# Optimization experiments

Measured on AMD Instinct MI355X. Metric: run time of the kernel, lower is better.

Reference implementation:

```python
import jax, jax.numpy as jnp
import numpy as np

NUM_BLOCKS = 6
D_MODEL = 1024
D_FF = 4096
NUM_HEADS = 16
NIN = 32
SEQ = NIN + 1  # +1 for SOS/EOS slot in the order-respecting mask
BATCH = 1024
D_HEAD = D_MODEL // NUM_HEADS
NEG = 1e10


def _order_masks(n):
    # order_respecting_mask with natural ordering arange(n)
    m0 = np.zeros((n + 1, n + 1), np.int32)  # input-layer mask
    m0[:, 0] = 1
    for s in range(n):
        for d in range(s + 1, n):
            m0[d, s + 1] = 1
    m0[-1, :] = 0
    mr = np.zeros((n + 1, n + 1), np.int32)  # later-layer mask (sees self)
    for s in range(n):
        for d in range(s, n):
            mr[d, s] = 1
    return jnp.asarray(m0), jnp.asarray(mr)


def setup_inputs() -> dict:
    key = jax.random.key(0)
    ks = jax.random.split(key, 6)
    std = 0.02  # Conv1d init std
    L, D, F = NUM_BLOCKS, D_MODEL, D_FF
    m0, mr = _order_masks(NIN)
    return {
        "x": jax.random.normal(ks[0], (BATCH, SEQ, D), jnp.float32),
        "qkv_w": std * jax.random.normal(ks[1], (L, D, 3 * D), jnp.float32),
        "qkv_b": jnp.zeros((L, 3 * D), jnp.float32),
        "proj_w": std * jax.random.normal(ks[2], (L, D, D), jnp.float32),
        "proj_b": jnp.zeros((L, D), jnp.float32),
        "w1": std * jax.random.normal(ks[3], (L, D, F), jnp.float32),
        "b1": jnp.zeros((L, F), jnp.float32),
        "w2": std * jax.random.normal(ks[4], (L, F, D), jnp.float32),
        "b2": jnp.zeros((L, D), jnp.float32),
        "ln1_s": jnp.ones((L, D), jnp.float32),
        "ln1_b": jnp.zeros((L, D), jnp.float32),
        "ln2_s": jnp.ones((L, D), jnp.float32),
        "ln2_b": jnp.zeros((L, D), jnp.float32),
        "lnf_s": jnp.ones((D,), jnp.float32),
        "lnf_b": jnp.zeros((D,), jnp.float32),
        "mask0": m0,
        "mask_rest": mr,
    }


def _ln(h, scale, shift, eps=1e-5):
    mean = h.mean(-1, keepdims=True)
    var = jnp.mean((h - mean) ** 2, axis=-1, keepdims=True)
    return scale * ((h - mean) * jax.lax.rsqrt(var + eps)) + shift


def _forward(x, qkv_w, qkv_b, proj_w, proj_b, w1, b1, w2, b2,
             ln1_s, ln1_b, ln2_s, ln2_b, lnf_s, lnf_b, mask0, mask_rest):
    B, S, D = x.shape
    H, Dh = NUM_HEADS, D_HEAD
    inv_sqrt_dk = 1.0 / np.sqrt(Dh).astype(np.float32)
    for l in range(qkv_w.shape[0]):
        m = (mask0 if l == 0 else mask_rest).astype(x.dtype)  # [S,S]
        h = _ln(x, ln1_s[l], ln1_b[l])
        qkv = h @ qkv_w[l] + qkv_b[l]  # [B,S,3D]
        q, k, v = [t.reshape(B, S, H, Dh) for t in jnp.split(qkv, 3, axis=-1)]
        scores = jnp.einsum('bshd,bthd->bhst', q, k) * inv_sqrt_dk  # [B,H,S,S]
        scores = scores * m - (1.0 - m) * NEG  # multiplicative+additive mask, as in source
        attn = jax.nn.softmax(scores, axis=-1)
        o = jnp.einsum('bhst,bthd->bshd', attn, v).reshape(B, S, D)
        x = x + (o @ proj_w[l] + proj_b[l])  # residual
        h = _ln(x, ln2_s[l], ln2_b[l])
        x = x + (jax.nn.gelu(h @ w1[l] + b1[l], approximate=False) @ w2[l] + b2[l])
    return _ln(x, lnf_s, lnf_b)  # ln_output=True


def reference(x, qkv_w, qkv_b, proj_w, proj_b, w1, b1, w2, b2,
              ln1_s, ln1_b, ln2_s, ln2_b, lnf_s, lnf_b, mask0, mask_rest):
    return _forward(x, qkv_w, qkv_b, proj_w, proj_b, w1, b1, w2, b2,
                    ln1_s, ln1_b, ln2_s, ln2_b, lnf_s, lnf_b, mask0, mask_rest)
```

## Files before the change

### kernel.cpp

```cpp
#include <hip/hip_runtime.h>

typedef unsigned short u16;
typedef __attribute__((ext_vector_type(8))) short s16x8;
typedef __attribute__((ext_vector_type(4))) float f32x4;

__device__ __forceinline__ float b2f(u16 u){ union{unsigned int i; float f;} v; v.i=((unsigned int)u)<<16; return v.f; }
__device__ __forceinline__ u16 f2b(float f){ union{float f; unsigned int i;} v; v.f=f; unsigned int r=v.i+0x7FFFu+((v.i>>16)&1u); return (u16)(r>>16); }

__device__ __forceinline__ void gload16(const void* g, void* l){
  __builtin_amdgcn_global_load_lds((const __attribute__((address_space(1))) void*)g,
                                   (__attribute__((address_space(3))) void*)l, 16, 0, 0);
}

__global__ void probe_k(const unsigned int* __restrict__ w, int* __restrict__ flag){
  if (threadIdx.x==0 && blockIdx.x==0) flag[0] = (w[0]!=0x3F800000u) ? 1 : 0;
}

__global__ __launch_bounds__(256) void conv2f32_k(const void* __restrict__ src, float* __restrict__ dst,
                                                  int n, const int* __restrict__ flag){
  const bool isb = flag[0]!=0;
  int i = (blockIdx.x*256+threadIdx.x)*4;
  for (int e=0;e<4;e++){
    int j=i+e;
    if (j<n) dst[j] = isb ? b2f(((const u16*)src)[j]) : ((const float*)src)[j];
  }
}

__global__ __launch_bounds__(256) void conv2bf16_k(const void* __restrict__ src, u16* __restrict__ dst,
                                                   int n, const int* __restrict__ flag){
  const bool isb = flag[0]!=0;
  int i = (blockIdx.x*256+threadIdx.x)*4;
  for (int e=0;e<4;e++){
    int j=i+e;
    if (j<n) dst[j] = isb ? ((const u16*)src)[j] : f2b(((const float*)src)[j]);
  }
}

__global__ __launch_bounds__(256) void transconv_k(const void* __restrict__ W, size_t ebase,
                                                   u16* __restrict__ Wt, int K, int Nc,
                                                   const int* __restrict__ flag){
  __shared__ float t[32][33];
  const bool isb = flag[0]!=0;
  const int n0 = blockIdx.x*32, k0 = blockIdx.y*32;
  const int tx = threadIdx.x, ty = threadIdx.y;
  #pragma unroll
  for (int r=0;r<4;r++){
    int row = ty + r*8;
    size_t idx = ebase + (size_t)(k0+row)*Nc + n0 + tx;
    t[row][tx] = isb ? b2f(((const u16*)W)[idx]) : ((const float*)W)[idx];
  }
  __syncthreads();
  #pragma unroll
  for (int r=0;r<4;r++){
    int row = ty + r*8;
    Wt[(size_t)(n0+row)*K + k0 + tx] = f2b(t[tx][row]);
  }
}

template<int XF32>
__global__ __launch_bounds__(256) void ln_k(const void* __restrict__ Xv, const float* __restrict__ sc,
                                            const float* __restrict__ sh, u16* __restrict__ O){
  const size_t t = blockIdx.x;
  const int tid = threadIdx.x;
  float x0,x1,x2,x3;
  if (XF32){
    float4 f = ((const float4*)Xv)[t*256 + tid];
    x0=f.x; x1=f.y; x2=f.z; x3=f.w;
  } else {
    uint2 u = *(const uint2*)((const u16*)Xv + t*1024 + tid*4);
    x0=b2f((u16)(u.x&0xFFFF)); x1=b2f((u16)(u.x>>16)); x2=b2f((u16)(u.y&0xFFFF)); x3=b2f((u16)(u.y>>16));
  }
  float s = x0+x1+x2+x3;
  float q = x0*x0+x1*x1+x2*x2+x3*x3;
  #pragma unroll
  for (int off=32; off; off>>=1){ s += __shfl_xor(s, off, 64); q += __shfl_xor(q, off, 64); }
  __shared__ float as[4], aq[4];
  if ((tid&63)==0){ as[tid>>6]=s; aq[tid>>6]=q; }
  __syncthreads();
  s = as[0]+as[1]+as[2]+as[3];
  q = aq[0]+aq[1]+aq[2]+aq[3];
  float mean = s*(1.0f/1024.0f);
  float var  = q*(1.0f/1024.0f) - mean*mean;
  float rs = rsqrtf(var + 1e-5f);
  int c = tid*4;
  float y0 = sc[c+0]*((x0-mean)*rs)+sh[c+0];
  float y1 = sc[c+1]*((x1-mean)*rs)+sh[c+1];
  float y2 = sc[c+2]*((x2-mean)*rs)+sh[c+2];
  float y3 = sc[c+3]*((x3-mean)*rs)+sh[c+3];
  uint2 o; o.x=(unsigned)f2b(y0)|((unsigned)f2b(y1)<<16); o.y=(unsigned)f2b(y2)|((unsigned)f2b(y3)<<16);
  *(uint2*)(O + t*1024 + tid*4) = o;
}

template<int XF32>
__global__ __launch_bounds__(256) void ln_out_k(const void* __restrict__ Xv, const float* __restrict__ sc,
                                                const float* __restrict__ sh, void* __restrict__ out,
                                                const int* __restrict__ flag){
  const size_t t = blockIdx.x;
  const int tid = threadIdx.x;
  float x0,x1,x2,x3;
  if (XF32){
    float4 f = ((const float4*)Xv)[t*256 + tid];
    x0=f.x; x1=f.y; x2=f.z; x3=f.w;
  } else {
    uint2 u = *(const uint2*)((const u16*)Xv + t*1024 + tid*4);
    x0=b2f((u16)(u.x&0xFFFF)); x1=b2f((u16)(u.x>>16)); x2=b2f((u16)(u.y&0xFFFF)); x3=b2f((u16)(u.y>>16));
  }
  float s = x0+x1+x2+x3;
  float q = x0*x0+x1*x1+x2*x2+x3*x3;
  #pragma unroll
  for (int off=32; off; off>>=1){ s += __shfl_xor(s, off, 64); q += __shfl_xor(q, off, 64); }
  __shared__ float as[4], aq[4];
  if ((tid&63)==0){ as[tid>>6]=s; aq[tid>>6]=q; }
  __syncthreads();
  s = as[0]+as[1]+as[2]+as[3];
  q = aq[0]+aq[1]+aq[2]+aq[3];
  float mean = s*(1.0f/1024.0f);
  float var  = q*(1.0f/1024.0f) - mean*mean;
  float rs = rsqrtf(var + 1e-5f);
  int c = tid*4;
  float y0 = sc[c+0]*((x0-mean)*rs)+sh[c+0];
  float y1 = sc[c+1]*((x1-mean)*rs)+sh[c+1];
  float y2 = sc[c+2]*((x2-mean)*rs)+sh[c+2];
  float y3 = sc[c+3]*((x3-mean)*rs)+sh[c+3];
  if (flag[0]){
    uint2 o; o.x=(unsigned)f2b(y0)|((unsigned)f2b(y1)<<16); o.y=(unsigned)f2b(y2)|((unsigned)f2b(y3)<<16);
    *(uint2*)((u16*)out + t*1024 + tid*4) = o;
  } else {
    float4 o4; o4.x=y0; o4.y=y1; o4.z=y2; o4.w=y3;
    ((float4*)out)[t*256 + tid] = o4;
  }
}

__global__ __launch_bounds__(128) void attn_k(const u16* __restrict__ QKV, const int* __restrict__ mask,
                                              u16* __restrict__ O){
  __shared__ float q[33][65];
  __shared__ float ks[33][65];
  __shared__ float vs[33][65];
  __shared__ float p[33][34];
  const int tid = threadIdx.x;
  const int b = blockIdx.x>>4, h = blockIdx.x&15;
  const size_t tok0 = (size_t)b*33;
  for (int idx=tid; idx<33*16; idx+=128){
    int s=idx>>4, d4=(idx&15)*4;
    size_t base=(tok0+s)*3072 + h*64 + d4;
    uint2 uq=*(const uint2*)(QKV+base);
    uint2 uk=*(const uint2*)(QKV+base+1024);
    uint2 uv=*(const uint2*)(QKV+base+2048);
    q[s][d4+0]=b2f((u16)(uq.x&0xFFFF)); q[s][d4+1]=b2f((u16)(uq.x>>16));
    q[s][d4+2]=b2f((u16)(uq.y&0xFFFF)); q[s][d4+3]=b2f((u16)(uq.y>>16));
    ks[s][d4+0]=b2f((u16)(uk.x&0xFFFF)); ks[s][d4+1]=b2f((u16)(uk.x>>16));
    ks[s][d4+2]=b2f((u16)(uk.y&0xFFFF)); ks[s][d4+3]=b2f((u16)(uk.y>>16));
    vs[s][d4+0]=b2f((u16)(uv.x&0xFFFF)); vs[s][d4+1]=b2f((u16)(uv.x>>16));
    vs[s][d4+2]=b2f((u16)(uv.y&0xFFFF)); vs[s][d4+3]=b2f((u16)(uv.y>>16));
  }
  __syncthreads();
  for (int idx=tid; idx<33*9; idx+=128){
    int s=idx/9, tg=idx-s*9;
    int t0=tg*4;
    float a0=0.f,a1=0.f,a2=0.f,a3=0.f;
    if (t0<=s && s<32){
      int t1=min(t0+1,32), t2=min(t0+2,32), t3=min(t0+3,32);
      #pragma unroll
      for (int d=0; d<64; d++){
        float qq=q[s][d];
        a0+=qq*ks[t0][d]; a1+=qq*ks[t1][d]; a2+=qq*ks[t2][d]; a3+=qq*ks[t3][d];
      }
    }
    float av[4]={a0,a1,a2,a3};
    #pragma unroll
    for (int e=0;e<4;e++){
      int t=t0+e;
      if (t<33) p[s][t] = mask[s*33+t] ? av[e]*0.125f : -1e10f;
    }
  }
  __syncthreads();
  if (tid<33){
    float mx=-3.4e38f;
    for (int t=0;t<33;t++) mx = fmaxf(mx, p[tid][t]);
    float sm=0.f;
    for (int t=0;t<33;t++){ float e=expf(p[tid][t]-mx); p[tid][t]=e; sm+=e; }
    float inv=1.0f/sm;
    for (int t=0;t<33;t++) p[tid][t]*=inv;
  }
  __syncthreads();
  for (int idx=tid; idx<33*16; idx+=128){
    int s=idx>>4, d4=(idx&15)*4;
    float a0=0.f,a1=0.f,a2=0.f,a3=0.f;
    for (int t=0;t<=s;t++){
      float pp=p[s][t];
      a0+=pp*vs[t][d4+0]; a1+=pp*vs[t][d4+1]; a2+=pp*vs[t][d4+2]; a3+=pp*vs[t][d4+3];
    }
    uint2 o; o.x=(unsigned)f2b(a0)|((unsigned)f2b(a1)<<16); o.y=(unsigned)f2b(a2)|((unsigned)f2b(a3)<<16);
    *(uint2*)(O + (tok0+s)*1024 + h*64 + d4) = o;
  }
}

template<int MODE>
__global__ __launch_bounds__(256) void gemm_k(const u16* __restrict__ A, const u16* __restrict__ Bt,
                                              const float* __restrict__ bias, void* __restrict__ Cv,
                                              int Nc, int K){
  __shared__ __align__(16) u16 As[128*64];
  __shared__ __align__(16) u16 Bs[128*64];
  const int tid = threadIdx.x;
  const int wave = tid>>6, lane = tid&63;

  const int gx = gridDim.x, gy = gridDim.y;
  int id = blockIdx.y*gx + blockIdx.x;
  const int nwg = gx*gy;
  const int q8 = nwg>>3, r8 = nwg&7;
  const int xcd = id&7; id >>= 3;
  const int nid = (xcd<r8 ? xcd*(q8+1) : r8*(q8+1)+(xcd-r8)*q8) + id;
  const int g   = nid / (4*gx);
  const int rem = nid - g*(4*gx);
  const int rows = min(4, gy - g*4);
  const int nb  = rem / rows;
  const int mi  = rem - nb*rows;
  const int m0  = (g*4 + mi)*128, n0 = nb*128;

  const int wm = (wave>>1)*64, wn = (wave&1)*64;
  const int r15 = lane&15, kg = lane>>4;
  f32x4 acc[4][4];
  #pragma unroll
  for (int i=0;i<4;i++)
    #pragma unroll
    for (int j=0;j<4;j++) acc[i][j] = (f32x4){0.f,0.f,0.f,0.f};

  for (int k0=0;k0<K;k0+=64){
    __syncthreads();
    #pragma unroll
    for (int i=0;i<4;i++){
      int c = tid + i*256;
      int r = c>>3, cc = c&7;
      int gcc = cc ^ (r&7);
      gload16(A  + (size_t)(m0+r)*K + k0 + gcc*8, As + (size_t)(i*256+wave*64)*8);
      gload16(Bt + (size_t)(n0+r)*K + k0 + gcc*8, Bs + (size_t)(i*256+wave*64)*8);
    }
    __syncthreads();
    #pragma unroll
    for (int ks=0;ks<2;ks++){
      s16x8 a[4], b[4];
      const int crd = ((ks*4+kg) ^ (r15&7))*8;
      #pragma unroll
      for (int i=0;i<4;i++) a[i] = *(const s16x8*)(As + (size_t)(wm + i*16 + r15)*64 + crd);
      #pragma unroll
      for (int j=0;j<4;j++) b[j] = *(const s16x8*)(Bs + (size_t)(wn + j*16 + r15)*64 + crd);
      #pragma unroll
      for (int i=0;i<4;i++)
        #pragma unroll
        for (int j=0;j<4;j++)
          acc[i][j] = __builtin_amdgcn_mfma_f32_16x16x32_bf16(a[i], b[j], acc[i][j], 0, 0, 0);
    }
  }
  #pragma unroll
  for (int i=0;i<4;i++){
    #pragma unroll
    for (int j=0;j<4;j++){
      int col = n0 + wn + j*16 + r15;
      float bc = bias[col];
      #pragma unroll
      for (int r=0;r<4;r++){
        int row = m0 + wm + i*16 + kg*4 + r;
        float vv = acc[i][j][r] + bc;
        if (MODE==1) vv = 0.5f*vv*(1.0f + erff(vv*0.70710678118f));
        size_t idx = (size_t)row*Nc + col;
        if (MODE==2){
          ((float*)Cv)[idx] += vv;
        } else if (MODE==3){
          u16* C = (u16*)Cv;
          C[idx] = f2b(vv + b2f(C[idx]));
        } else {
          ((u16*)Cv)[idx] = f2b(vv);
        }
      }
    }
  }
}

extern "C" void kernel_launch(void* const* d_in, const int* in_sizes, int n_in,
                              void* d_out, int out_size, void* d_ws, size_t ws_size,
                              hipStream_t stream){
  (void)in_sizes; (void)n_in; (void)out_size;
  const int L=6, D=1024, TD=3072, F=4096, NTOK=1024*33;
  const size_t PARAMN = 81920;

  auto need = [&](int xf32, int mc)->size_t{
    size_t t=0;
    auto add=[&](size_t b){ t=(t+255)&~(size_t)255; t+=b; };
    add((size_t)NTOK*D*(xf32?4:2)); add(PARAMN*4); add(4);
    add((size_t)mc*D*2); add((size_t)mc*F*2);
    add((size_t)TD*D*2); add((size_t)D*D*2); add((size_t)F*D*2); add((size_t)D*F*2);
    return t;
  };
  int xf32 = 1, mc = NTOK;
  if (ws_size < need(1,NTOK)){
    mc = 16896;
    if (ws_size < need(1,16896)){
      mc = 8448;
      if (ws_size < need(1,8448)) xf32 = 0;
    }
  }
  const int nch = NTOK/mc;

  char* basep = (char*)d_ws; size_t off=0;
  auto alloc=[&](size_t b)->char*{ off=(off+255)&~(size_t)255; char* p=basep+off; off+=b; return p; };
  void*  X   = (void*)alloc((size_t)NTOK*D*(xf32?4:2));
  float* pf  = (float*)alloc(PARAMN*4);
  int*   flag= (int*)alloc(4);
  u16*   H   = (u16*)alloc((size_t)mc*D*2);
  u16*   BIG = (u16*)alloc((size_t)mc*F*2);
  u16*   wQ  = (u16*)alloc((size_t)TD*D*2);
  u16*   wP  = (u16*)alloc((size_t)D*D*2);
  u16*   w1  = (u16*)alloc((size_t)F*D*2);
  u16*   w2  = (u16*)alloc((size_t)D*F*2);

  const size_t pQB=0, pPB=pQB+(size_t)L*TD, pB1=pPB+(size_t)L*D, pB2=pB1+(size_t)L*F,
               pL1S=pB2+(size_t)L*D, pL1B=pL1S+(size_t)L*D, pL2S=pL1B+(size_t)L*D,
               pL2B=pL2S+(size_t)L*D, pLFS=pL2B+(size_t)L*D, pLFB=pLFS+D;

  probe_k<<<1,64,0,stream>>>((const unsigned int*)d_in[9], flag);
  if (xf32) conv2f32_k<<<(NTOK*D)/1024,256,0,stream>>>(d_in[0], (float*)X, NTOK*D, flag);
  else      conv2bf16_k<<<(NTOK*D)/1024,256,0,stream>>>(d_in[0], (u16*)X, NTOK*D, flag);
  {
    struct PRM { int idx; size_t offe; int n; };
    const PRM prm[10] = {
      {2,pQB,L*TD},{4,pPB,L*D},{6,pB1,L*F},{8,pB2,L*D},
      {9,pL1S,L*D},{10,pL1B,L*D},{11,pL2S,L*D},{12,pL2B,L*D},
      {13,pLFS,D},{14,pLFB,D}};
    for (int i=0;i<10;i++)
      conv2f32_k<<<(prm[i].n+1023)/1024,256,0,stream>>>(d_in[prm[i].idx], pf+prm[i].offe, prm[i].n, flag);
  }

  const size_t xstride = (size_t)D*(xf32?4:2);
  for (int l=0;l<L;l++){
    transconv_k<<<dim3(TD/32, D/32), dim3(32,8),0,stream>>>(d_in[1], (size_t)l*D*TD, wQ, D, TD, flag);
    transconv_k<<<dim3(D/32,  D/32), dim3(32,8),0,stream>>>(d_in[3], (size_t)l*D*D,  wP, D, D,  flag);
    transconv_k<<<dim3(F/32,  D/32), dim3(32,8),0,stream>>>(d_in[5], (size_t)l*D*F,  w1, D, F,  flag);
    transconv_k<<<dim3(D/32,  F/32), dim3(32,8),0,stream>>>(d_in[7], (size_t)l*F*D,  w2, F, D,  flag);
    const int* msk = (const int*)d_in[l==0?15:16];
    for (int c=0;c<nch;c++){
      void* Xc = (void*)((char*)X + (size_t)c*mc*xstride);
      if (xf32) ln_k<1><<<mc,256,0,stream>>>(Xc, pf+pL1S+(size_t)l*D, pf+pL1B+(size_t)l*D, H);
      else      ln_k<0><<<mc,256,0,stream>>>(Xc, pf+pL1S+(size_t)l*D, pf+pL1B+(size_t)l*D, H);
      gemm_k<0><<<dim3(TD/128, mc/128),256,0,stream>>>(H, wQ, pf+pQB+(size_t)l*TD, BIG, TD, D);
      attn_k<<<(mc/33)*16,128,0,stream>>>(BIG, msk, H);
      if (xf32) gemm_k<2><<<dim3(D/128, mc/128),256,0,stream>>>(H, wP, pf+pPB+(size_t)l*D, Xc, D, D);
      else      gemm_k<3><<<dim3(D/128, mc/128),256,0,stream>>>(H, wP, pf+pPB+(size_t)l*D, Xc, D, D);
      if (xf32) ln_k<1><<<mc,256,0,stream>>>(Xc, pf+pL2S+(size_t)l*D, pf+pL2B+(size_t)l*D, H);
      else      ln_k<0><<<mc,256,0,stream>>>(Xc, pf+pL2S+(size_t)l*D, pf+pL2B+(size_t)l*D, H);
      gemm_k<1><<<dim3(F/128, mc/128),256,0,stream>>>(H, w1, pf+pB1+(size_t)l*F, BIG, F, D);
      if (xf32) gemm_k<2><<<dim3(D/128, mc/128),256,0,stream>>>(BIG, w2, pf+pB2+(size_t)l*D, Xc, D, F);
      else      gemm_k<3><<<dim3(D/128, mc/128),256,0,stream>>>(BIG, w2, pf+pB2+(size_t)l*D, Xc, D, F);
    }
  }
  if (xf32) ln_out_k<1><<<NTOK,256,0,stream>>>(X, pf+pLFS, pf+pLFB, d_out, flag);
  else      ln_out_k<0><<<NTOK,256,0,stream>>>(X, pf+pLFS, pf+pLFB, d_out, flag);
}
```

Before: 9.944 ms.

## Add LDS-free direct-load GEMM with register double buffering for FFN

Adds a GEMM variant that loads A and B fragments straight from global memory into registers, skipping shared memory and block barriers. It double-buffers the two 32-wide K halves so loads overlap the MFMA work. It is used for both FFN GEMMs. Without LDS sharing, each wave fetches its operand rows itself, so reuse across waves depends on the caches and global traffic may rise. Register pressure also goes up.

Result: slower. 17.35 ms (+74.5%).

```diff
diff --git a/kernel.cpp b/kernel.cpp
--- a/kernel.cpp
+++ b/kernel.cpp
@@ -195,16 +195,7 @@
   }
 }
 
-template<int MODE>
-__global__ __launch_bounds__(256) void gemm_k(const u16* __restrict__ A, const u16* __restrict__ Bt,
-                                              const float* __restrict__ bias, void* __restrict__ Cv,
-                                              int Nc, int K){
-  __shared__ __align__(16) u16 As[128*64];
-  __shared__ __align__(16) u16 Bs[128*64];
-  const int tid = threadIdx.x;
-  const int wave = tid>>6, lane = tid&63;
-
-  const int gx = gridDim.x, gy = gridDim.y;
+__device__ __forceinline__ void remap_mn(int gx, int gy, int& m0, int& n0){
   int id = blockIdx.y*gx + blockIdx.x;
   const int nwg = gx*gy;
   const int q8 = nwg>>3, r8 = nwg&7;
@@ -215,8 +206,18 @@
   const int rows = min(4, gy - g*4);
   const int nb  = rem / rows;
   const int mi  = rem - nb*rows;
-  const int m0  = (g*4 + mi)*128, n0 = nb*128;
-
+  m0 = (g*4 + mi)*128; n0 = nb*128;
+}
+
+template<int MODE>
+__global__ __launch_bounds__(256) void gemm_k(const u16* __restrict__ A, const u16* __restrict__ Bt,
+                                              const float* __restrict__ bias, void* __restrict__ Cv,
+                                              int Nc, int K){
+  __shared__ __align__(16) u16 As[128*64];
+  __shared__ __align__(16) u16 Bs[128*64];
+  const int tid = threadIdx.x;
+  const int wave = tid>>6, lane = tid&63;
+  int m0, n0; remap_mn(gridDim.x, gridDim.y, m0, n0);
   const int wm = (wave>>1)*64, wn = (wave&1)*64;
   const int r15 = lane&15, kg = lane>>4;
   f32x4 acc[4][4];
@@ -251,6 +252,74 @@
           acc[i][j] = __builtin_amdgcn_mfma_f32_16x16x32_bf16(a[i], b[j], acc[i][j], 0, 0, 0);
     }
   }
+  #pragma unroll
+  for (int i=0;i<4;i++){
+    #pragma unroll
+    for (int j=0;j<4;j++){
+      int col = n0 + wn + j*16 + r15;
+      float bc = bias[col];
+      #pragma unroll
+      for (int r=0;r<4;r++){
+        int row = m0 + wm + i*16 + kg*4 + r;
+        float vv = acc[i][j][r] + bc;
+        if (MODE==1) vv = 0.5f*vv*(1.0f + erff(vv*0.70710678118f));
+        size_t idx = (size_t)row*Nc + col;
+        if (MODE==2){
+          ((float*)Cv)[idx] += vv;
+        } else if (MODE==3){
+          u16* C = (u16*)Cv;
+          C[idx] = f2b(vv + b2f(C[idx]));
+        } else {
+          ((u16*)Cv)[idx] = f2b(vv);
+        }
+      }
+    }
+  }
+}
+
+template<int MODE>
+__global__ __launch_bounds__(256) void gemmd_k(const u16* __restrict__ A, const u16* __restrict__ Bt,
+                                               const float* __restrict__ bias, void* __restrict__ Cv,
+                                               int Nc, int K){
+  const int tid = threadIdx.x;
+  const int wave = tid>>6, lane = tid&63;
+  int m0, n0; remap_mn(gridDim.x, gridDim.y, m0, n0);
+  const int wm = (wave>>1)*64, wn = (wave&1)*64;
+  const int r15 = lane&15, kg = lane>>4;
+
+  const u16* Ab = A  + (size_t)(m0+wm+r15)*K + kg*8;
+  const u16* Bb = Bt + (size_t)(n0+wn+r15)*K + kg*8;
+
+  f32x4 acc[4][4];
+  #pragma unroll
+  for (int i=0;i<4;i++)
+    #pragma unroll
+    for (int j=0;j<4;j++) acc[i][j] = (f32x4){0.f,0.f,0.f,0.f};
+
+  s16x8 aA[4], bA[4], aB[4], bB[4];
+  auto LD = [&](s16x8* a, s16x8* b, int k0){
+    #pragma unroll
+    for (int i=0;i<4;i++) a[i] = *(const s16x8*)(Ab + (size_t)i*16*K + k0);
+    #pragma unroll
+    for (int j=0;j<4;j++) b[j] = *(const s16x8*)(Bb + (size_t)j*16*K + k0);
+  };
+  auto FM = [&](s16x8* a, s16x8* b){
+    #pragma unroll
+    for (int i=0;i<4;i++)
+      #pragma unroll
+      for (int j=0;j<4;j++)
+        acc[i][j] = __builtin_amdgcn_mfma_f32_16x16x32_bf16(a[i], b[j], acc[i][j], 0, 0, 0);
+  };
+
+  const int NT = K>>6;
+  LD(aA, bA, 0);
+  for (int t=0;t<NT;t++){
+    LD(aB, bB, t*64+32);
+    FM(aA, bA);
+    if (t+1<NT) LD(aA, bA, (t+1)*64);
+    FM(aB, bB);
+  }
+
   #pragma unroll
   for (int i=0;i<4;i++){
     #pragma unroll
@@ -347,9 +416,9 @@
       else      gemm_k<3><<<dim3(D/128, mc/128),256,0,stream>>>(H, wP, pf+pPB+(size_t)l*D, Xc, D, D);
       if (xf32) ln_k<1><<<mc,256,0,stream>>>(Xc, pf+pL2S+(size_t)l*D, pf+pL2B+(size_t)l*D, H);
       else      ln_k<0><<<mc,256,0,stream>>>(Xc, pf+pL2S+(size_t)l*D, pf+pL2B+(size_t)l*D, H);
-      gemm_k<1><<<dim3(F/128, mc/128),256,0,stream>>>(H, w1, pf+pB1+(size_t)l*F, BIG, F, D);
-      if (xf32) gemm_k<2><<<dim3(D/128, mc/128),256,0,stream>>>(BIG, w2, pf+pB2+(size_t)l*D, Xc, D, F);
-      else      gemm_k<3><<<dim3(D/128, mc/128),256,0,stream>>>(BIG, w2, pf+pB2+(size_t)l*D, Xc, D, F);
+      gemmd_k<1><<<dim3(F/128, mc/128),256,0,stream>>>(H, w1, pf+pB1+(size_t)l*F, BIG, F, D);
+      if (xf32) gemmd_k<2><<<dim3(D/128, mc/128),256,0,stream>>>(BIG, w2, pf+pB2+(size_t)l*D, Xc, D, F);
+      else      gemmd_k<3><<<dim3(D/128, mc/128),256,0,stream>>>(BIG, w2, pf+pB2+(size_t)l*D, Xc, D, F);
     }
   }
   if (xf32) ln_out_k<1><<<NTOK,256,0,stream>>>(X, pf+pLFS, pf+pLFB, d_out, flag);
```
